# Optimization experiments

Hardware: AMD Instinct MI355X
Metric: run time of the kernel (lower is better)

## Reference

```python
import jax, jax.numpy as jnp
import numpy as np

N = 20000          # nodes
E = 320000         # edges (before self loops)
IN_DIM = 64
HID = 128
HEADS = 4
LAYERS = 3
GRAPHS = 64
NEG_SLOPE = 0.2
LN_EPS = 1e-5


def setup_inputs() -> dict:
    key = jax.random.key(0)
    ks = jax.random.split(key, 12)
    x = jax.random.normal(ks[0], (N, IN_DIM), dtype=jnp.float32)
    edge_index = jax.random.randint(ks[1], (2, E), 0, N, dtype=jnp.int64)
    batch = jnp.sort(jax.random.randint(ks[2], (N,), 0, GRAPHS, dtype=jnp.int64))
    s = 0.05
    W_in = jax.random.normal(ks[3], (IN_DIM, HID), dtype=jnp.float32) * s
    b_in = jnp.zeros((HID,), dtype=jnp.float32)
    Ws = jax.random.normal(ks[4], (LAYERS, HID, HEADS * HID), dtype=jnp.float32) * s
    att_src = jax.random.normal(ks[5], (LAYERS, HEADS, HID), dtype=jnp.float32) * s
    att_dst = jax.random.normal(ks[6], (LAYERS, HEADS, HID), dtype=jnp.float32) * s
    conv_b = jnp.zeros((LAYERS, HID), dtype=jnp.float32)
    ln_g = jnp.ones((LAYERS, HID), dtype=jnp.float32)
    ln_b = jnp.zeros((LAYERS, HID), dtype=jnp.float32)
    return {"x": x, "edge_index": edge_index, "batch": batch,
            "W_in": W_in, "b_in": b_in, "Ws": Ws, "att_src": att_src,
            "att_dst": att_dst, "conv_b": conv_b, "ln_g": ln_g, "ln_b": ln_b}


def _gat_layer(x, src, dst, W, a_src, a_dst, bias):
    # x: [N, HID] -> h: [N, HEADS, HID]
    h = (x @ W).reshape(N, HEADS, HID)
    alpha_s = jnp.einsum('nhc,hc->nh', h, a_src)   # [N, H]
    alpha_d = jnp.einsum('nhc,hc->nh', h, a_dst)   # [N, H]
    e = jax.nn.leaky_relu(alpha_s[src] + alpha_d[dst], NEG_SLOPE)  # [E', H]
    # segment softmax over destination node (every node has a self loop)
    m = jax.ops.segment_max(e, dst, num_segments=N)
    e = jnp.exp(e - m[dst])
    denom = jax.ops.segment_sum(e, dst, num_segments=N)
    a = e / (denom[dst] + 1e-16)                    # [E', H]
    msg = h[src] * a[:, :, None]                    # [E', H, HID]
    out = jax.ops.segment_sum(msg, dst, num_segments=N)  # [N, H, HID]
    return out.mean(axis=1) + bias                  # concat=False -> head mean


def _layer_norm(x, g, b):
    mu = x.mean(axis=-1, keepdims=True)
    var = ((x - mu) ** 2).mean(axis=-1, keepdims=True)
    return (x - mu) * jax.lax.rsqrt(var + LN_EPS) * g + b


def reference(x, edge_index, batch, W_in, b_in, Ws, att_src, att_dst, conv_b, ln_g, ln_b):
    # add self loops (PyG GATConv default)
    loops = jnp.arange(N, dtype=edge_index.dtype)
    src = jnp.concatenate([edge_index[0], loops])
    dst = jnp.concatenate([edge_index[1], loops])

    h = x @ W_in + b_in
    for l in range(LAYERS):
        conv = _gat_layer(h, src, dst, Ws[l], att_src[l], att_dst[l], conv_b[l])
        h = _layer_norm(jax.nn.relu(conv) + h, ln_g[l], ln_b[l])

    # global mean pool over graphs
    sums = jax.ops.segment_sum(h, batch, num_segments=GRAPHS)
    cnt = jax.ops.segment_sum(jnp.ones((N,), dtype=h.dtype), batch, num_segments=GRAPHS)
    return sums / jnp.maximum(cnt, 1.0)[:, None]
```

## Files before the change

kernel.cpp:

```cpp
#include <hip/hip_runtime.h>
#include <hip/hip_bf16.h>
#include <math.h>

#define N_NODES 20000
#define N_EDGES 320000
#define IN_DIM 64
#define HID 128
#define HEADS 4
#define LAYERS 3
#define GRAPHS 64
#define TOT_E (N_EDGES + N_NODES)
#define NEG_SLOPE 0.2f
#define LN_EPS 1e-5f
#define MAXD 96
#define OB 132

typedef __attribute__((ext_vector_type(8))) short short8v;
typedef __attribute__((ext_vector_type(4))) float f32x4;
typedef __attribute__((ext_vector_type(2))) float f32x2;


__global__ void zero_kernel(int* __restrict__ cursor) {
    int i = blockIdx.x * blockDim.x + threadIdx.x;
    if (i < N_NODES) cursor[i] = 0;
}

__global__ void fill_slots(const int* __restrict__ ei, int* __restrict__ cursor,
                           int* __restrict__ slots) {
    int e = blockIdx.x * blockDim.x + threadIdx.x;
    if (e >= TOT_E) return;
    int src, dst;
    if (e < N_EDGES) { src = ei[e]; dst = ei[N_EDGES + e]; }
    else { src = e - N_EDGES; dst = src; }
    int pos = atomicAdd(&cursor[dst], 1);
    if (pos < MAXD) slots[dst * MAXD + pos] = src;
}


#define NV (LAYERS * 128 * 512)
#define NWIN (HID * IN_DIM)
#define NX (N_NODES * IN_DIM)
#define NU (LAYERS * HEADS * HID)

__global__ void pack_all(const float* __restrict__ Ws, const float* __restrict__ W_in,
                         const float* __restrict__ x, const float* __restrict__ att_src,
                         const float* __restrict__ att_dst,
                         __hip_bfloat16* __restrict__ Vt, __hip_bfloat16* __restrict__ Wt_in,
                         __hip_bfloat16* __restrict__ xb,
                         float* __restrict__ u_s, float* __restrict__ u_d) {
    int i = blockIdx.x * blockDim.x + threadIdx.x;
    if (i < NV) {
        int l = i / 65536;
        int r = i % 65536;
        int c = r / 512, hk = r % 512;
        int hh = hk >> 7, k = hk & 127;
        Vt[i] = __float2bfloat16(0.25f * Ws[(size_t)l * 65536 + k * 512 + hh * 128 + c]);
    } else if (i < NV + NWIN) {
        int r = i - NV;
        int n = r / 64, k = r % 64;
        Wt_in[r] = __float2bfloat16(W_in[k * 128 + n]);
    } else if (i < NV + NWIN + NX) {
        int r = i - NV - NWIN;
        xb[r] = __float2bfloat16(x[r]);
    } else if (i < NV + NWIN + NX + NU) {
        int t = i - NV - NWIN - NX;
        int l = t / 512;
        int r = t % 512;
        int hh = r / 128, k = r % 128;
        const float* wrow = Ws + (size_t)l * 65536 + k * 512 + hh * 128;
        const float* as = att_src + l * 512 + hh * 128;
        const float* ad = att_dst + l * 512 + hh * 128;
        float ss = 0.f, sd = 0.f;
        for (int c = 0; c < 128; ++c) {
            float w = wrow[c];
            ss = fmaf(w, as[c], ss);
            sd = fmaf(w, ad[c], sd);
        }
        u_s[t] = ss; u_d[t] = sd;
    }
}


__global__ __launch_bounds__(256) void gemm_in(
    const __hip_bfloat16* __restrict__ Ax,
    const __hip_bfloat16* __restrict__ Bt,
    const float* __restrict__ bias,
    const float* __restrict__ u_s0, const float* __restrict__ u_d0,
    float* __restrict__ h, unsigned char* __restrict__ h8,
    float* __restrict__ a_s, float* __restrict__ a_d) {
    __shared__ __hip_bfloat16 As[64 * 64];
    const int M_ = N_NODES;
    int tid = threadIdx.x;
    int lane = tid & 63, w = tid >> 6;
    int lr = lane & 15, lg = lane >> 4;
    int row0 = blockIdx.x * 64;
#pragma unroll
    for (int it = 0; it < 2; ++it) {
        int chunk = it * 256 + tid;
        int row = chunk >> 3, c8 = chunk & 7;
        int sc = c8 ^ (row & 7);
        int gr = row0 + row; if (gr >= M_) gr = M_ - 1;
        const __hip_bfloat16* src = Ax + (size_t)gr * 64 + sc * 8;
        __builtin_amdgcn_global_load_lds(
            (const void __attribute__((address_space(1)))*)src,
            (void __attribute__((address_space(3)))*)(As + chunk * 8), 16, 0, 0);
    }
    __syncthreads();

    f32x4 acc[8] = {};
    int rl = w * 16 + lr;
#pragma unroll
    for (int ks = 0; ks < 2; ++ks) {
        int kc = ks * 4 + lg;
        short8v a = *(const short8v*)&As[(rl * 8 + (kc ^ (rl & 7))) * 8];
#pragma unroll
        for (int nf = 0; nf < 8; ++nf) {
            short8v b = *(const short8v*)&Bt[(size_t)(nf * 16 + lr) * 64 + ks * 32 + lg * 8];
            acc[nf] = __builtin_amdgcn_mfma_f32_16x16x32_bf16(a, b, acc[nf], 0, 0, 0);
        }
    }

    float cb[8], us[4][8], ud[4][8];
#pragma unroll
    for (int nf = 0; nf < 8; ++nf) cb[nf] = bias[nf * 16 + lr];
#pragma unroll
    for (int hh = 0; hh < 4; ++hh)
#pragma unroll
        for (int nf = 0; nf < 8; ++nf) {
            us[hh][nf] = u_s0[hh * 128 + nf * 16 + lr];
            ud[hh][nf] = u_d0[hh * 128 + nf * 16 + lr];
        }

#pragma unroll
    for (int j = 0; j < 4; ++j) {
        int r = row0 + w * 16 + lg * 4 + j;
        if (r >= M_) continue;
        float vals[8];
#pragma unroll
        for (int nf = 0; nf < 8; ++nf) {
            float v = acc[nf][j] + cb[nf];
            vals[nf] = v;
            h[(size_t)r * HID + nf * 16 + lr] = v;
            int d = __builtin_amdgcn_cvt_pk_fp8_f32(v, v, 0, false);
            h8[(size_t)r * HID + nf * 16 + lr] = (unsigned char)(d & 0xff);
        }
#pragma unroll
        for (int hh = 0; hh < 4; ++hh) {
            float ps = 0.f, pd = 0.f;
#pragma unroll
            for (int nf = 0; nf < 8; ++nf) {
                ps = fmaf(vals[nf], us[hh][nf], ps);
                pd = fmaf(vals[nf], ud[hh][nf], pd);
            }
            ps += __shfl_xor(ps, 1); pd += __shfl_xor(pd, 1);
            ps += __shfl_xor(ps, 2); pd += __shfl_xor(pd, 2);
            ps += __shfl_xor(ps, 4); pd += __shfl_xor(pd, 4);
            ps += __shfl_xor(ps, 8); pd += __shfl_xor(pd, 8);
            if (lr == 0) { a_s[r * 4 + hh] = ps; a_d[r * 4 + hh] = pd; }
        }
    }
}


__global__ __launch_bounds__(256) void layer_fused(
    const int* __restrict__ deg_arr, const int* __restrict__ slots,
    const unsigned char* __restrict__ h8i, const float* __restrict__ a_si,
    const float* __restrict__ a_di,
    const __hip_bfloat16* __restrict__ Vt,
    const float* __restrict__ conv_b, const float* __restrict__ ln_g,
    const float* __restrict__ ln_b,
    const float* __restrict__ u_sn, const float* __restrict__ u_dn,
    float* __restrict__ h, unsigned char* __restrict__ h8o,
    float* __restrict__ a_so, float* __restrict__ a_do, int last) {
    __shared__ __attribute__((aligned(16))) __hip_bfloat16 aggLds[16 * 512];
    __shared__ __attribute__((aligned(16))) char uMem[16 * OB * 4];
    float* outb = (float*)uMem;
    float (*eLds)[MAXD * 4] = (float(*)[MAXD * 4])uMem;
    int (*sLds)[MAXD] = (int(*)[MAXD])(uMem + 4 * MAXD * 4 * 4);

    int tid = threadIdx.x;
    int lane = tid & 63, wv = tid >> 6;
    int row0 = blockIdx.x * 16;
    int hh = lane >> 4;
    int j  = lane & 15;
    const unsigned char* hbase = h8i + j * 8;

    for (int t = 0; t < 4; ++t) {
        int row = wv * 4 + t;
        int n = row0 + row;
        int deg = deg_arr[n]; if (deg > MAXD) deg = MAXD;
        int beg = n * MAXD;

        int ja = lane >> 2, ha = lane & 3;
        float adh = a_di[n * 4 + ha];
        float mx = -3.4e38f;
        for (int c = 0; c < deg; c += 16) {
            int idx = c + ja;
            float e = -3.4e38f;
            if (idx < deg) {
                int s = slots[beg + idx];
                if (ha == 0) sLds[wv][idx] = s;
                e = a_si[s * 4 + ha] + adh;
                e = (e > 0.f) ? e : NEG_SLOPE * e;
            }
            eLds[wv][idx * 4 + ha] = e;
            mx = fmaxf(mx, e);
        }
        mx = fmaxf(mx, __shfl_xor(mx, 4));
        mx = fmaxf(mx, __shfl_xor(mx, 8));
        mx = fmaxf(mx, __shfl_xor(mx, 16));
        mx = fmaxf(mx, __shfl_xor(mx, 32));
        float dsum = 0.f;
        for (int c = 0; c < deg; c += 16) {
            int idx = c + ja;
            if (idx < deg) {
                float p = __expf(eLds[wv][idx * 4 + ha] - mx);
                eLds[wv][idx * 4 + ha] = p;
                dsum += p;
            }
        }
        dsum += __shfl_xor(dsum, 4);
        dsum += __shfl_xor(dsum, 8);
        dsum += __shfl_xor(dsum, 16);
        dsum += __shfl_xor(dsum, 32);
        float dh = __shfl(dsum, hh);
        float inv_own = 1.f / (dh + 1e-16f);

        float acc[8] = {0.f, 0.f, 0.f, 0.f, 0.f, 0.f, 0.f, 0.f};
        int i = 0;
        for (; i + 3 < deg; i += 4) {
            int ss[4]; float pp[4]; uint2 uu[4];
#pragma unroll
            for (int k = 0; k < 4; ++k) {
                ss[k] = sLds[wv][i + k];
                pp[k] = eLds[wv][(i + k) * 4 + hh];
            }
#pragma unroll
            for (int k = 0; k < 4; ++k)
                uu[k] = *(const uint2*)(hbase + (size_t)ss[k] * HID);
#pragma unroll
            for (int k = 0; k < 4; ++k) {
                f32x2 a01 = __builtin_amdgcn_cvt_pk_f32_fp8(uu[k].x, false);
                f32x2 a23 = __builtin_amdgcn_cvt_pk_f32_fp8(uu[k].x, true);
                f32x2 a45 = __builtin_amdgcn_cvt_pk_f32_fp8(uu[k].y, false);
                f32x2 a67 = __builtin_amdgcn_cvt_pk_f32_fp8(uu[k].y, true);
                acc[0] = fmaf(pp[k], a01[0], acc[0]);
                acc[1] = fmaf(pp[k], a01[1], acc[1]);
                acc[2] = fmaf(pp[k], a23[0], acc[2]);
                acc[3] = fmaf(pp[k], a23[1], acc[3]);
                acc[4] = fmaf(pp[k], a45[0], acc[4]);
                acc[5] = fmaf(pp[k], a45[1], acc[5]);
                acc[6] = fmaf(pp[k], a67[0], acc[6]);
                acc[7] = fmaf(pp[k], a67[1], acc[7]);
            }
        }
        for (; i < deg; ++i) {
            int s0 = sLds[wv][i];
            float p0 = eLds[wv][i * 4 + hh];
            uint2 u0 = *(const uint2*)(hbase + (size_t)s0 * HID);
            f32x2 a01 = __builtin_amdgcn_cvt_pk_f32_fp8(u0.x, false);
            f32x2 a23 = __builtin_amdgcn_cvt_pk_f32_fp8(u0.x, true);
            f32x2 a45 = __builtin_amdgcn_cvt_pk_f32_fp8(u0.y, false);
            f32x2 a67 = __builtin_amdgcn_cvt_pk_f32_fp8(u0.y, true);
            acc[0] = fmaf(p0, a01[0], acc[0]);
            acc[1] = fmaf(p0, a01[1], acc[1]);
            acc[2] = fmaf(p0, a23[0], acc[2]);
            acc[3] = fmaf(p0, a23[1], acc[3]);
            acc[4] = fmaf(p0, a45[0], acc[4]);
            acc[5] = fmaf(p0, a45[1], acc[5]);
            acc[6] = fmaf(p0, a67[0], acc[6]);
            acc[7] = fmaf(p0, a67[1], acc[7]);
        }

        __hip_bfloat162 q[4];
#pragma unroll
        for (int k = 0; k < 4; ++k) {
            q[k].x = __float2bfloat16(acc[2 * k] * inv_own);
            q[k].y = __float2bfloat16(acc[2 * k + 1] * inv_own);
        }
        *(uint4*)&aggLds[row * 512 + (16 * hh + (j ^ row)) * 8] = *(uint4*)q;
    }
    __syncthreads();

    int lr = lane & 15, lg = lane >> 4;
    f32x4 macc[2] = {};
    const __hip_bfloat16* Bb0 = Vt + (size_t)(wv * 32 + lr) * 512;
    const __hip_bfloat16* Bb1 = Vt + (size_t)(wv * 32 + 16 + lr) * 512;
#pragma unroll
    for (int ks = 0; ks < 16; ++ks) {
        int kc = ks * 4 + lg;
        int pos = (kc & ~15) | ((kc & 15) ^ lr);
        short8v a = *(const short8v*)&aggLds[lr * 512 + pos * 8];
        int ko = ks * 32 + lg * 8;
        short8v b0 = *(const short8v*)(Bb0 + ko);
        short8v b1 = *(const short8v*)(Bb1 + ko);
        macc[0] = __builtin_amdgcn_mfma_f32_16x16x32_bf16(a, b0, macc[0], 0, 0, 0);
        macc[1] = __builtin_amdgcn_mfma_f32_16x16x32_bf16(a, b1, macc[1], 0, 0, 0);
    }
    __syncthreads();
#pragma unroll
    for (int nf = 0; nf < 2; ++nf)
#pragma unroll
        for (int jj = 0; jj < 4; ++jj)
            outb[(lg * 4 + jj) * OB + wv * 32 + nf * 16 + lr] = macc[nf][jj];
    __syncthreads();

    int row = tid >> 4, q = tid & 15;
    int r = row0 + row;
    int c0 = q * 8;
    float v[8];
#pragma unroll
    for (int c = 0; c < 8; ++c) v[c] = outb[row * OB + c0 + c];

    float4 cb0 = *(const float4*)&conv_b[c0];
    float4 cb1 = *(const float4*)&conv_b[c0 + 4];
    float cb[8] = {cb0.x, cb0.y, cb0.z, cb0.w, cb1.x, cb1.y, cb1.z, cb1.w};
    float4 h0 = *(const float4*)&h[(size_t)r * HID + c0];
    float4 h1 = *(const float4*)&h[(size_t)r * HID + c0 + 4];
    float hr[8] = {h0.x, h0.y, h0.z, h0.w, h1.x, h1.y, h1.z, h1.w};
    float s1 = 0.f;
#pragma unroll
    for (int c = 0; c < 8; ++c) {
        v[c] = fmaxf(v[c] + cb[c], 0.f) + hr[c];
        s1 += v[c];
    }
    s1 += __shfl_xor(s1, 1); s1 += __shfl_xor(s1, 2);
    s1 += __shfl_xor(s1, 4); s1 += __shfl_xor(s1, 8);
    float mu = s1 * (1.f / HID);
    float s2 = 0.f;
#pragma unroll
    for (int c = 0; c < 8; ++c) {
        v[c] -= mu;
        s2 += v[c] * v[c];
    }
    s2 += __shfl_xor(s2, 1); s2 += __shfl_xor(s2, 2);
    s2 += __shfl_xor(s2, 4); s2 += __shfl_xor(s2, 8);
    float rstd = rsqrtf(s2 * (1.f / HID) + LN_EPS);
    float4 g0 = *(const float4*)&ln_g[c0];
    float4 g1 = *(const float4*)&ln_g[c0 + 4];
    float4 b0 = *(const float4*)&ln_b[c0];
    float4 b1 = *(const float4*)&ln_b[c0 + 4];
    float gg[8] = {g0.x, g0.y, g0.z, g0.w, g1.x, g1.y, g1.z, g1.w};
    float bb[8] = {b0.x, b0.y, b0.z, b0.w, b1.x, b1.y, b1.z, b1.w};
    float o[8];
#pragma unroll
    for (int c = 0; c < 8; ++c) o[c] = v[c] * rstd * gg[c] + bb[c];

    *(float4*)&h[(size_t)r * HID + c0] = make_float4(o[0], o[1], o[2], o[3]);
    *(float4*)&h[(size_t)r * HID + c0 + 4] = make_float4(o[4], o[5], o[6], o[7]);
    int d0 = 0, d1 = 0;
    d0 = __builtin_amdgcn_cvt_pk_fp8_f32(o[0], o[1], d0, false);
    d0 = __builtin_amdgcn_cvt_pk_fp8_f32(o[2], o[3], d0, true);
    d1 = __builtin_amdgcn_cvt_pk_fp8_f32(o[4], o[5], d1, false);
    d1 = __builtin_amdgcn_cvt_pk_fp8_f32(o[6], o[7], d1, true);
    *(uint2*)&h8o[(size_t)r * HID + c0] = make_uint2((unsigned)d0, (unsigned)d1);

    if (!last) {
#pragma unroll
        for (int ah = 0; ah < 4; ++ah) {
            float4 usa = *(const float4*)&u_sn[ah * 128 + c0];
            float4 usb = *(const float4*)&u_sn[ah * 128 + c0 + 4];
            float4 uda = *(const float4*)&u_dn[ah * 128 + c0];
            float4 udb = *(const float4*)&u_dn[ah * 128 + c0 + 4];
            float ps = o[0] * usa.x + o[1] * usa.y + o[2] * usa.z + o[3] * usa.w +
                       o[4] * usb.x + o[5] * usb.y + o[6] * usb.z + o[7] * usb.w;
            float pd = o[0] * uda.x + o[1] * uda.y + o[2] * uda.z + o[3] * uda.w +
                       o[4] * udb.x + o[5] * udb.y + o[6] * udb.z + o[7] * udb.w;
            ps += __shfl_xor(ps, 1); pd += __shfl_xor(pd, 1);
            ps += __shfl_xor(ps, 2); pd += __shfl_xor(pd, 2);
            ps += __shfl_xor(ps, 4); pd += __shfl_xor(pd, 4);
            ps += __shfl_xor(ps, 8); pd += __shfl_xor(pd, 8);
            if (q == 0) { a_so[r * 4 + ah] = ps; a_do[r * 4 + ah] = pd; }
        }
    }
}


__global__ __launch_bounds__(128) void pool2_kernel(
    const float* __restrict__ h, const int* __restrict__ batch,
    float* __restrict__ out) {
    int g = blockIdx.x;
    int c = threadIdx.x;
    __shared__ int sLo, sHi;
    if (c == 0) {
        int lo = 0, hi = N_NODES;
        while (lo < hi) { int m = (lo + hi) >> 1; if (batch[m] < g) lo = m + 1; else hi = m; }
        sLo = lo;
        hi = N_NODES;
        while (lo < hi) { int m = (lo + hi) >> 1; if (batch[m] < g + 1) lo = m + 1; else hi = m; }
        sHi = lo;
    }
    __syncthreads();
    int lo = sLo, hi = sHi;
    float s[8] = {0.f, 0.f, 0.f, 0.f, 0.f, 0.f, 0.f, 0.f};
    int n = lo;
    for (; n + 7 < hi; n += 8) {
#pragma unroll
        for (int k = 0; k < 8; ++k)
            s[k] += h[(size_t)(n + k) * HID + c];
    }
    for (; n < hi; ++n) s[0] += h[(size_t)n * HID + c];
    float sum = ((s[0] + s[1]) + (s[2] + s[3])) + ((s[4] + s[5]) + (s[6] + s[7]));
    int cnt = hi - lo; if (cnt < 1) cnt = 1;
    out[g * HID + c] = sum / (float)cnt;
}


extern "C" void kernel_launch(void* const* d_in, const int* in_sizes, int n_in,
                              void* d_out, int out_size, void* d_ws, size_t ws_size,
                              hipStream_t stream) {
    const float* x      = (const float*)d_in[0];
    const int*   ei     = (const int*)d_in[1];
    const int*   batch  = (const int*)d_in[2];
    const float* W_in   = (const float*)d_in[3];
    const float* b_in   = (const float*)d_in[4];
    const float* Ws     = (const float*)d_in[5];
    const float* att_src= (const float*)d_in[6];
    const float* att_dst= (const float*)d_in[7];
    const float* conv_b = (const float*)d_in[8];
    const float* ln_g   = (const float*)d_in[9];
    const float* ln_b   = (const float*)d_in[10];
    float* out = (float*)d_out;

    char* ws = (char*)d_ws;
    size_t off = 0;
    auto alloc = [&](size_t bytes) -> void* {
        void* p = ws + off;
        off = (off + bytes + 255) & ~(size_t)255;
        return p;
    };
    float* h            = (float*)alloc((size_t)N_NODES * HID * 4);
    unsigned char* h8a  = (unsigned char*)alloc((size_t)N_NODES * HID);
    unsigned char* h8b  = (unsigned char*)alloc((size_t)N_NODES * HID);
    __hip_bfloat16* Vt  = (__hip_bfloat16*)alloc((size_t)NV * 2);
    __hip_bfloat16* Wti = (__hip_bfloat16*)alloc((size_t)NWIN * 2);
    __hip_bfloat16* xb  = (__hip_bfloat16*)alloc((size_t)NX * 2);
    float* u_s    = (float*)alloc((size_t)NU * 4);
    float* u_d    = (float*)alloc((size_t)NU * 4);
    float* a_sa   = (float*)alloc((size_t)N_NODES * HEADS * 4);
    float* a_sb   = (float*)alloc((size_t)N_NODES * HEADS * 4);
    float* a_da   = (float*)alloc((size_t)N_NODES * HEADS * 4);
    float* a_db   = (float*)alloc((size_t)N_NODES * HEADS * 4);
    int* cursor   = (int*)alloc(N_NODES * 4);
    int* slots    = (int*)alloc((size_t)N_NODES * MAXD * 4);

    zero_kernel<<<(N_NODES + 255) / 256, 256, 0, stream>>>(cursor);
    fill_slots<<<(TOT_E + 255) / 256, 256, 0, stream>>>(ei, cursor, slots);
    pack_all<<<(NV + NWIN + NX + NU + 255) / 256, 256, 0, stream>>>(
        Ws, W_in, x, att_src, att_dst, Vt, Wti, xb, u_s, u_d);

    gemm_in<<<(N_NODES + 63) / 64, 256, 0, stream>>>(
        xb, Wti, b_in, u_s, u_d, h, h8a, a_sa, a_da);

    unsigned char* h8bufs[2] = {h8a, h8b};
    float* asbufs[2] = {a_sa, a_sb};
    float* adbufs[2] = {a_da, a_db};
    for (int l = 0; l < LAYERS; ++l) {
        int cur = l & 1, nxt = (l + 1) & 1;
        int lu = (l + 1 < LAYERS) ? l + 1 : l;
        layer_fused<<<N_NODES / 16, 256, 0, stream>>>(
            cursor, slots, h8bufs[cur], asbufs[cur], adbufs[cur],
            Vt + (size_t)l * 65536,
            conv_b + (size_t)l * HID, ln_g + (size_t)l * HID, ln_b + (size_t)l * HID,
            u_s + (size_t)lu * 512, u_d + (size_t)lu * 512,
            h, h8bufs[nxt], asbufs[nxt], adbufs[nxt], (l == LAYERS - 1) ? 1 : 0);
    }

    pool2_kernel<<<GRAPHS, 128, 0, stream>>>(h, batch, out);
}
```

Baseline: 206.2 us.

## Double-buffer next node's edge logits to overlap with current aggregation

Result: no change. 205.6 us (-0.3%).

```diff
diff --git a/kernel.cpp b/kernel.cpp
--- a/kernel.cpp
+++ b/kernel.cpp
@@ -12,7 +12,7 @@
 #define TOT_E (N_EDGES + N_NODES)
 #define NEG_SLOPE 0.2f
 #define LN_EPS 1e-5f
-#define MAXD 96
+#define MAXD 64
 #define OB 132
 
 typedef __attribute__((ext_vector_type(8))) short short8v;
@@ -173,39 +173,45 @@
     float* __restrict__ h, unsigned char* __restrict__ h8o,
     float* __restrict__ a_so, float* __restrict__ a_do, int last) {
     __shared__ __attribute__((aligned(16))) __hip_bfloat16 aggLds[16 * 512];
-    __shared__ __attribute__((aligned(16))) char uMem[16 * OB * 4];
+    __shared__ __attribute__((aligned(16))) char uMem[10240];
     float* outb = (float*)uMem;
-    float (*eLds)[MAXD * 4] = (float(*)[MAXD * 4])uMem;
-    int (*sLds)[MAXD] = (int(*)[MAXD])(uMem + 4 * MAXD * 4 * 4);
+    float (*eLds)[2][MAXD * 4] = (float(*)[2][MAXD * 4])uMem;
+    int (*sLds)[2][MAXD] = (int(*)[2][MAXD])(uMem + 8192);
 
     int tid = threadIdx.x;
     int lane = tid & 63, wv = tid >> 6;
     int row0 = blockIdx.x * 16;
     int hh = lane >> 4;
     int j  = lane & 15;
+    int ja = lane >> 2, ha = lane & 3;
     const unsigned char* hbase = h8i + j * 8;
 
-    for (int t = 0; t < 4; ++t) {
-        int row = wv * 4 + t;
-        int n = row0 + row;
-        int deg = deg_arr[n]; if (deg > MAXD) deg = MAXD;
-        int beg = n * MAXD;
-
-        int ja = lane >> 2, ha = lane & 3;
-        float adh = a_di[n * 4 + ha];
-        float mx = -3.4e38f;
+    float mxNext = -3.4e38f;
+    {
+        int n0 = row0 + wv * 4;
+        int deg = deg_arr[n0]; if (deg > MAXD) deg = MAXD;
+        int beg = n0 * MAXD;
+        float adh = a_di[n0 * 4 + ha];
         for (int c = 0; c < deg; c += 16) {
             int idx = c + ja;
             float e = -3.4e38f;
             if (idx < deg) {
                 int s = slots[beg + idx];
-                if (ha == 0) sLds[wv][idx] = s;
+                if (ha == 0) sLds[wv][0][idx] = s;
                 e = a_si[s * 4 + ha] + adh;
                 e = (e > 0.f) ? e : NEG_SLOPE * e;
             }
-            eLds[wv][idx * 4 + ha] = e;
-            mx = fmaxf(mx, e);
-        }
+            eLds[wv][0][idx * 4 + ha] = e;
+            mxNext = fmaxf(mxNext, e);
+        }
+    }
+
+    for (int t = 0; t < 4; ++t) {
+        int buf = t & 1;
+        int n = row0 + wv * 4 + t;
+        int deg = deg_arr[n]; if (deg > MAXD) deg = MAXD;
+
+        float mx = mxNext;
         mx = fmaxf(mx, __shfl_xor(mx, 4));
         mx = fmaxf(mx, __shfl_xor(mx, 8));
         mx = fmaxf(mx, __shfl_xor(mx, 16));
@@ -214,8 +220,8 @@
         for (int c = 0; c < deg; c += 16) {
             int idx = c + ja;
             if (idx < deg) {
-                float p = __expf(eLds[wv][idx * 4 + ha] - mx);
-                eLds[wv][idx * 4 + ha] = p;
+                float p = __expf(eLds[wv][buf][idx * 4 + ha] - mx);
+                eLds[wv][buf][idx * 4 + ha] = p;
                 dsum += p;
             }
         }
@@ -226,14 +232,34 @@
         float dh = __shfl(dsum, hh);
         float inv_own = 1.f / (dh + 1e-16f);
 
+        if (t < 3) {
+            int n1 = n + 1;
+            int deg1 = deg_arr[n1]; if (deg1 > MAXD) deg1 = MAXD;
+            int beg1 = n1 * MAXD;
+            float adh1 = a_di[n1 * 4 + ha];
+            mxNext = -3.4e38f;
+            for (int c = 0; c < deg1; c += 16) {
+                int idx = c + ja;
+                float e = -3.4e38f;
+                if (idx < deg1) {
+                    int s = slots[beg1 + idx];
+                    if (ha == 0) sLds[wv][buf ^ 1][idx] = s;
+                    e = a_si[s * 4 + ha] + adh1;
+                    e = (e > 0.f) ? e : NEG_SLOPE * e;
+                }
+                eLds[wv][buf ^ 1][idx * 4 + ha] = e;
+                mxNext = fmaxf(mxNext, e);
+            }
+        }
+
         float acc[8] = {0.f, 0.f, 0.f, 0.f, 0.f, 0.f, 0.f, 0.f};
         int i = 0;
         for (; i + 3 < deg; i += 4) {
             int ss[4]; float pp[4]; uint2 uu[4];
 #pragma unroll
             for (int k = 0; k < 4; ++k) {
-                ss[k] = sLds[wv][i + k];
-                pp[k] = eLds[wv][(i + k) * 4 + hh];
+                ss[k] = sLds[wv][buf][i + k];
+                pp[k] = eLds[wv][buf][(i + k) * 4 + hh];
             }
 #pragma unroll
             for (int k = 0; k < 4; ++k)
@@ -255,8 +281,8 @@
             }
         }
         for (; i < deg; ++i) {
-            int s0 = sLds[wv][i];
-            float p0 = eLds[wv][i * 4 + hh];
+            int s0 = sLds[wv][buf][i];
+            float p0 = eLds[wv][buf][i * 4 + hh];
             uint2 u0 = *(const uint2*)(hbase + (size_t)s0 * HID);
             f32x2 a01 = __builtin_amdgcn_cvt_pk_f32_fp8(u0.x, false);
             f32x2 a23 = __builtin_amdgcn_cvt_pk_f32_fp8(u0.x, true);
@@ -272,6 +298,7 @@
             acc[7] = fmaf(p0, a67[1], acc[7]);
         }
 
+        int row = wv * 4 + t;
         __hip_bfloat162 q[4];
 #pragma unroll
         for (int k = 0; k < 4; ++k) {
```
